# Kernel tuning notes

Hardware: AMD Instinct MI355X
Metric: run time of the kernel (lower is better)

Reference implementation:

```python
import jax, jax.numpy as jnp
import numpy as np

B, T, D, H = 2, 2048, 1024, 16
HD = D // H            # 64
FH = 2752              # SwiGLU hidden: round64(int(2*4*D/3))
BETA_INIT = 0.5


def rmsnorm(x, w, eps=1e-6):
    x32 = x.astype(jnp.float32)
    r = jax.lax.rsqrt(jnp.mean(x32 * x32, axis=-1, keepdims=True) + eps)
    return (x32 * r).astype(x.dtype) * w


def rope(x, cos, sin):
    # x: (B,H,T,HD); cos/sin: (T,HD//2)
    d2 = x.shape[-1] // 2
    x1, x2 = x[..., :d2], x[..., d2:]
    return jnp.concatenate([x1 * cos - x2 * sin, x2 * cos + x1 * sin], axis=-1)


def delta_res(x, h, gn_w, g_w, g_b, wv_w, eps_k=1e-6):
    # k-hat = normalize(h); k = k_hat / sqrt(d)
    h32 = h.astype(jnp.float32)
    nrm = jnp.sqrt(jnp.sum(h32 * h32, axis=-1, keepdims=True))
    k = (h32 / jnp.maximum(nrm, eps_k)).astype(x.dtype) * (1.0 / np.sqrt(D))
    c = rmsnorm(x, gn_w)
    logit = c @ g_w + g_b                                   # (B,T)
    beta = (2.0 * jax.nn.sigmoid(logit.astype(jnp.float32))).astype(x.dtype)[..., None]
    v = jax.nn.sigmoid(x @ wv_w)[..., None]                 # (B,T,1)
    kTx = jnp.sum(k * x, axis=-1, keepdims=True)
    return x + beta * (v - kTx) * k


def setup_inputs() -> dict:
    key = jax.random.key(0)
    ks = jax.random.split(key, 12)
    s = 0.02
    gb = np.float32(np.log(BETA_INIT / 2.0 / (1.0 - BETA_INIT / 2.0 + 1e-8)))
    return {
        "x": jax.random.normal(ks[0], (B, T, D), jnp.float32),
        "wq": jax.random.normal(ks[1], (D, D), jnp.float32) * s,
        "wk": jax.random.normal(ks[2], (D, D), jnp.float32) * s,
        "wv": jax.random.normal(ks[3], (D, D), jnp.float32) * s,
        "wo": jax.random.normal(ks[4], (D, D), jnp.float32) * s,
        "qn_w": jnp.ones((HD,), jnp.float32),
        "kn_w": jnp.ones((HD,), jnp.float32),
        "attn_norm_w": jnp.ones((D,), jnp.float32),
        "g1_norm_w": jnp.ones((D,), jnp.float32),
        "g1_w": jax.random.normal(ks[5], (D,), jnp.float32) * s,
        "g1_b": jnp.asarray(gb),
        "wv1": jax.random.normal(ks[6], (D,), jnp.float32) * s,
        "mlp_norm_w": jnp.ones((D,), jnp.float32),
        "w1": jax.random.normal(ks[7], (FH, D), jnp.float32) * s,
        "w2": jax.random.normal(ks[8], (D, FH), jnp.float32) * s,
        "w3": jax.random.normal(ks[9], (FH, D), jnp.float32) * s,
        "g2_norm_w": jnp.ones((D,), jnp.float32),
        "g2_w": jax.random.normal(ks[10], (D,), jnp.float32) * s,
        "g2_b": jnp.asarray(gb),
        "wv2": jax.random.normal(ks[11], (D,), jnp.float32) * s,
    }


def reference(x, wq, wk, wv, wo, qn_w, kn_w, attn_norm_w,
              g1_norm_w, g1_w, g1_b, wv1, mlp_norm_w, w1, w2, w3,
              g2_norm_w, g2_w, g2_b, wv2):
    # ---- attention sublayer (pre-norm) ----
    xc = rmsnorm(x, attn_norm_w)
    q = (xc @ wq.T).reshape(B, T, H, HD).swapaxes(1, 2)   # (B,H,T,HD)
    k = (xc @ wk.T).reshape(B, T, H, HD).swapaxes(1, 2)
    v = (xc @ wv.T).reshape(B, T, H, HD).swapaxes(1, 2)
    q = rmsnorm(q, qn_w)
    k = rmsnorm(k, kn_w)
    inv_freq = 1.0 / (10000.0 ** (jnp.arange(0, HD, 2, dtype=jnp.float32) / HD))
    freqs = jnp.arange(T, dtype=jnp.float32)[:, None] * inv_freq[None, :]  # (T,HD/2)
    cos, sin = jnp.cos(freqs), jnp.sin(freqs)
    q = rope(q, cos, sin)
    k = rope(k, cos, sin)
    scale = 1.0 / np.sqrt(HD)
    scores = jnp.einsum('bhqd,bhkd->bhqk', q, k) * scale
    causal = jnp.where(jnp.arange(T)[:, None] >= jnp.arange(T)[None, :], 0.0, -jnp.inf).astype(scores.dtype)
    attn = jax.nn.softmax(scores + causal, axis=-1)
    out = jnp.einsum('bhqk,bhkd->bhqd', attn, v)
    h_attn = out.swapaxes(1, 2).reshape(B, T, D) @ wo.T
    x = delta_res(x, h_attn, g1_norm_w, g1_w, g1_b, wv1)
    # ---- MLP sublayer (pre-norm SwiGLU) ----
    xm = rmsnorm(x, mlp_norm_w)
    h_mlp = (jax.nn.silu(xm @ w1.T) * (xm @ w3.T)) @ w2.T
    x = delta_res(x, h_mlp, g2_norm_w, g2_w, g2_b, wv2)
    return x
```

## Files before the change

kernel.cpp:

```cpp
#include <hip/hip_runtime.h>
#include <hip/hip_bf16.h>
#include <math.h>

using bf16 = __hip_bfloat16;
typedef __bf16 bf16x8 __attribute__((ext_vector_type(8)));
typedef float f32x4 __attribute__((ext_vector_type(4)));

static constexpr int B_ = 2, T_ = 2048, D_ = 1024, H_ = 16, HD_ = 64, FH_ = 2752;
static constexpr int BT = B_ * T_;

struct __align__(8)  bh4 { bf16 h[4]; };
struct __align__(16) bh8 { bf16 h[8]; };

#define DEV static __device__ __forceinline__

DEV float b2f(bf16 v) { return __bfloat162float(v); }
DEV bf16  f2b(float v) { return __float2bfloat16(v); }
DEV __bf16 f2bb(float f) { __hip_bfloat16 h = __float2bfloat16(f); return *reinterpret_cast<__bf16*>(&h); }
DEV float sigmoidf_(float x) { return 1.0f / (1.0f + __expf(-x)); }

DEV void load4f(const bf16* p, float* v) {
    bh4 t = *reinterpret_cast<const bh4*>(p);
#pragma unroll
    for (int i = 0; i < 4; ++i) v[i] = b2f(t.h[i]);
}
DEV void load4f(const float* p, float* v) {
    float4 t = *reinterpret_cast<const float4*>(p);
    v[0] = t.x; v[1] = t.y; v[2] = t.z; v[3] = t.w;
}
DEV void store4(float* p, const float* v) {
    float4 t; t.x = v[0]; t.y = v[1]; t.z = v[2]; t.w = v[3];
    *reinterpret_cast<float4*>(p) = t;
}
DEV float waveReduceSum(float v) {
#pragma unroll
    for (int m = 32; m; m >>= 1) v += __shfl_xor(v, m);
    return v;
}

DEV void gl_lds16(const bf16* g, bf16* lds_base) {
    __builtin_amdgcn_global_load_lds(
        (const __attribute__((address_space(1))) void*)g,
        (__attribute__((address_space(3))) void*)lds_base, 16, 0, 0);
}

__global__ __launch_bounds__(256) void k_rope_tables(float* __restrict__ cost, float* __restrict__ sint) {
    int idx = blockIdx.x * 256 + threadIdx.x;
    if (idx >= T_ * 32) return;
    int t = idx >> 5, j = idx & 31;
    float inv = powf(10000.0f, -(float)j * (1.0f / 32.0f));
    float f = (float)t * inv;
    cost[idx] = cosf(f);
    sint[idx] = sinf(f);
}

__global__ __launch_bounds__(256) void k_f2b(const float* __restrict__ in, bf16* __restrict__ out, int n8) {
    int i = blockIdx.x * 256 + threadIdx.x;
    if (i >= n8) return;
    const float4* p = reinterpret_cast<const float4*>(in + (size_t)i * 8);
    float4 a = p[0], b = p[1];
    bh8 o;
    o.h[0] = f2b(a.x); o.h[1] = f2b(a.y); o.h[2] = f2b(a.z); o.h[3] = f2b(a.w);
    o.h[4] = f2b(b.x); o.h[5] = f2b(b.y); o.h[6] = f2b(b.z); o.h[7] = f2b(b.w);
    *reinterpret_cast<bh8*>(out + (size_t)i * 8) = o;
}

__global__ __launch_bounds__(256) void k_f2b_pair(const float* __restrict__ w1, const float* __restrict__ w3,
                                                  bf16* __restrict__ outp, int n8tot) {
    int i = blockIdx.x * 256 + threadIdx.x;
    if (i >= n8tot) return;
    int r = i >> 7, c8 = i & 127;
    int sel = (r >> 4) & 1;
    int j = ((r >> 5) << 4) | (r & 15);
    const float* src = (sel ? w3 : w1) + (size_t)j * D_ + c8 * 8;
    float4 a = reinterpret_cast<const float4*>(src)[0];
    float4 b = reinterpret_cast<const float4*>(src)[1];
    bh8 o;
    o.h[0] = f2b(a.x); o.h[1] = f2b(a.y); o.h[2] = f2b(a.z); o.h[3] = f2b(a.w);
    o.h[4] = f2b(b.x); o.h[5] = f2b(b.y); o.h[6] = f2b(b.z); o.h[7] = f2b(b.w);
    *reinterpret_cast<bh8*>(outp + (size_t)r * D_ + c8 * 8) = o;
}

__global__ __launch_bounds__(256) void k_rmsnorm(const float* __restrict__ x, const float* __restrict__ w,
                                                 bf16* __restrict__ out) {
    int row = blockIdx.x, tid = threadIdx.x;
    const float* xr = x + (size_t)row * D_;
    int base = tid * 4;
    float v[4];
    load4f(xr + base, v);
    float ss = v[0]*v[0] + v[1]*v[1] + v[2]*v[2] + v[3]*v[3];
    ss = waveReduceSum(ss);
    __shared__ float red[4];
    if ((tid & 63) == 0) red[tid >> 6] = ss;
    __syncthreads();
    ss = red[0] + red[1] + red[2] + red[3];
    float r = rsqrtf(ss * (1.0f / D_) + 1e-6f);
    float wv[4];
    load4f(w + base, wv);
    bh4 o;
#pragma unroll
    for (int i = 0; i < 4; ++i) o.h[i] = f2b(v[i] * r * wv[i]);
    *reinterpret_cast<bh4*>(out + (size_t)row * D_ + base) = o;
}

template <int EPI>
__global__ __launch_bounds__(512) void k_gemm256(const bf16* __restrict__ A, const bf16* __restrict__ W,
                                                 bf16* __restrict__ C, int M, int N, int K) {
    __shared__ bf16 sA[2][256 * 32];
    __shared__ bf16 sB[2][128 * 32];
    int tid = threadIdx.x, lane = tid & 63, wid = tid >> 6;
    int m0 = blockIdx.x * 256, n0 = blockIdx.y * 128;
    int wr = wid >> 1, wc = wid & 1;
    int l16 = lane & 15, lg = lane >> 4;
    int srow = lane >> 2;
    int scol = ((lane & 3) ^ ((lane >> 3) & 3)) * 8;
    int rchunk = (lg ^ ((l16 >> 1) & 3)) * 8;

    f32x4 acc[4][4] = {};

#define STAGE(buf, k0)                                                                   \
    {                                                                                    \
        _Pragma("unroll")                                                                \
        for (int c = 0; c < 2; ++c) {                                                    \
            int r0 = wid * 32 + c * 16;                                                  \
            gl_lds16(&A[(size_t)(m0 + r0 + srow) * K + (k0) + scol], &sA[buf][r0 * 32]); \
        }                                                                                \
        {                                                                                \
            int r0 = wid * 16;                                                           \
            gl_lds16(&W[(size_t)(n0 + r0 + srow) * K + (k0) + scol], &sB[buf][r0 * 32]); \
        }                                                                                \
    }

    int nk = K >> 5;
    STAGE(0, 0);
    if (nk > 1) STAGE(1, 32);
    for (int t = 0; t < nk; ++t) {
        if (t + 1 < nk) { asm volatile("s_waitcnt vmcnt(3)" ::: "memory"); }
        else            { asm volatile("s_waitcnt vmcnt(0)" ::: "memory"); }
        __builtin_amdgcn_s_barrier();
        __builtin_amdgcn_sched_barrier(0);
        int cur = t & 1;
        bf16x8 af[4], bfr[4];
#pragma unroll
        for (int m = 0; m < 4; ++m)
            af[m] = *reinterpret_cast<const bf16x8*>(&sA[cur][(wr * 64 + m * 16 + l16) * 32 + rchunk]);
#pragma unroll
        for (int n = 0; n < 4; ++n)
            bfr[n] = *reinterpret_cast<const bf16x8*>(&sB[cur][(wc * 64 + n * 16 + l16) * 32 + rchunk]);
        __builtin_amdgcn_s_setprio(1);
#pragma unroll
        for (int m = 0; m < 4; ++m)
#pragma unroll
            for (int n = 0; n < 4; ++n)
                acc[m][n] = __builtin_amdgcn_mfma_f32_16x16x32_bf16(af[m], bfr[n], acc[m][n], 0, 0, 0);
        __builtin_amdgcn_s_setprio(0);
        __builtin_amdgcn_sched_barrier(0);
        __builtin_amdgcn_s_barrier();
        if (t + 2 < nk) STAGE(cur, (t + 2) * 32);
    }
#undef STAGE

    int rbase = m0 + wr * 64;
    if (EPI == 1) {
        int Ng = N >> 1;
        int gbase = (n0 >> 1) + wc * 32;
#pragma unroll
        for (int m = 0; m < 4; ++m) {
#pragma unroll
            for (int n2 = 0; n2 < 2; ++n2) {
                int gcol = gbase + n2 * 16 + l16;
#pragma unroll
                for (int r = 0; r < 4; ++r) {
                    int row = rbase + m * 16 + lg * 4 + r;
                    float a1 = acc[m][n2 * 2][r];
                    float a3 = acc[m][n2 * 2 + 1][r];
                    C[(size_t)row * Ng + gcol] = f2b(a1 * sigmoidf_(a1) * a3);
                }
            }
        }
    } else {
        int cbase = n0 + wc * 64;
#pragma unroll
        for (int m = 0; m < 4; ++m) {
#pragma unroll
            for (int n = 0; n < 4; ++n) {
                int col = cbase + n * 16 + l16;
#pragma unroll
                for (int r = 0; r < 4; ++r) {
                    int row = rbase + m * 16 + lg * 4 + r;
                    C[(size_t)row * N + col] = f2b(acc[m][n][r]);
                }
            }
        }
    }
}

__global__ __launch_bounds__(256) void k_gemm64(const bf16* __restrict__ A, const bf16* __restrict__ W,
                                                bf16* __restrict__ C, int M, int N, int K) {
    __shared__ bf16 sA[2][128 * 32];
    __shared__ bf16 sB[2][64 * 32];
    int tid = threadIdx.x, lane = tid & 63, wid = tid >> 6;
    int m0 = blockIdx.x * 128, n0 = blockIdx.y * 64;
    int wr = wid;
    int l16 = lane & 15, lg = lane >> 4;
    int srow = lane >> 2;
    int scol = ((lane & 3) ^ ((lane >> 3) & 3)) * 8;
    int rchunk = (lg ^ ((l16 >> 1) & 3)) * 8;

    f32x4 acc[2][4] = {};

#define STAGE(buf, k0)                                                                   \
    {                                                                                    \
        _Pragma("unroll")                                                                \
        for (int c = 0; c < 2; ++c) {                                                    \
            int r0 = wid * 32 + c * 16;                                                  \
            gl_lds16(&A[(size_t)(m0 + r0 + srow) * K + (k0) + scol], &sA[buf][r0 * 32]); \
        }                                                                                \
        {                                                                                \
            int r0 = wid * 16;                                                           \
            gl_lds16(&W[(size_t)(n0 + r0 + srow) * K + (k0) + scol], &sB[buf][r0 * 32]); \
        }                                                                                \
    }

    int nk = K >> 5;
    STAGE(0, 0);
    if (nk > 1) STAGE(1, 32);
    for (int t = 0; t < nk; ++t) {
        if (t + 1 < nk) { asm volatile("s_waitcnt vmcnt(3)" ::: "memory"); }
        else            { asm volatile("s_waitcnt vmcnt(0)" ::: "memory"); }
        __builtin_amdgcn_s_barrier();
        __builtin_amdgcn_sched_barrier(0);
        int cur = t & 1;
        bf16x8 af[2], bfr[4];
#pragma unroll
        for (int m = 0; m < 2; ++m)
            af[m] = *reinterpret_cast<const bf16x8*>(&sA[cur][(wr * 32 + m * 16 + l16) * 32 + rchunk]);
#pragma unroll
        for (int n = 0; n < 4; ++n)
            bfr[n] = *reinterpret_cast<const bf16x8*>(&sB[cur][(n * 16 + l16) * 32 + rchunk]);
        __builtin_amdgcn_s_setprio(1);
#pragma unroll
        for (int m = 0; m < 2; ++m)
#pragma unroll
            for (int n = 0; n < 4; ++n)
                acc[m][n] = __builtin_amdgcn_mfma_f32_16x16x32_bf16(af[m], bfr[n], acc[m][n], 0, 0, 0);
        __builtin_amdgcn_s_setprio(0);
        __builtin_amdgcn_sched_barrier(0);
        __builtin_amdgcn_s_barrier();
        if (t + 2 < nk) STAGE(cur, (t + 2) * 32);
    }
#undef STAGE

    int rbase = m0 + wid * 32;
#pragma unroll
    for (int m = 0; m < 2; ++m) {
#pragma unroll
        for (int n = 0; n < 4; ++n) {
            int col = n0 + n * 16 + l16;
#pragma unroll
            for (int r = 0; r < 4; ++r) {
                int row = rbase + m * 16 + lg * 4 + r;
                C[(size_t)row * N + col] = f2b(acc[m][n][r]);
            }
        }
    }
}

__global__ __launch_bounds__(256) void k_qk_norm_rope(const bf16* __restrict__ qin, const float* __restrict__ wn,
                                                      const float* __restrict__ cost, const float* __restrict__ sint,
                                                      bf16* __restrict__ qout, float scale, int ld, int off) {
    int tid = threadIdx.x;
    int g = blockIdx.x * 4 + (tid >> 6);
    int d = tid & 63;
    int h = g % H_, t = (g / H_) % T_, b = g / (H_ * T_);
    float v = b2f(qin[(size_t)(b * T_ + t) * ld + off + h * HD_ + d]);
    float ss = waveReduceSum(v * v);
    float r = rsqrtf(ss * (1.0f / HD_) + 1e-6f);
    float xn = v * r * wn[d];
    float p = __shfl_xor(xn, 32);
    float c = cost[t * 32 + (d & 31)], s = sint[t * 32 + (d & 31)];
    float o = (d < 32) ? (xn * c - p * s) : (xn * c + p * s);
    qout[((size_t)(b * H_ + h) * T_ + t) * HD_ + d] = f2b(o * scale);
}

__global__ __launch_bounds__(256) void k_v_transpose(const bf16* __restrict__ vin, bf16* __restrict__ vt,
                                                     int ld, int off) {
    __shared__ bf16 tile[64][72];
    int tid = threadIdx.x;
    int bh = blockIdx.y;
    int t0 = blockIdx.x * 64;
    int b = bh >> 4, h = bh & 15;
#pragma unroll
    for (int i = 0; i < 16; ++i) {
        int lin = i * 256 + tid;
        int tl = lin >> 6, d = lin & 63;
        tile[tl][d] = vin[(size_t)(b * T_ + t0 + tl) * ld + off + h * HD_ + d];
    }
    __syncthreads();
#pragma unroll
    for (int i = 0; i < 16; ++i) {
        int lin = i * 256 + tid;
        int d = lin >> 6, tl = lin & 63;
        vt[((size_t)bh * HD_ + d) * T_ + t0 + tl] = tile[tl][d];
    }
}

template <bool MASKED>
DEV void fa3_tile(const bf16* __restrict__ kl, const bf16* __restrict__ vl,
                  int l16, int lg, int qloc,
                  const bf16x8 qf0, const bf16x8 qf1,
                  f32x4* acc, float& m_r, float& l_r) {
    f32x4 s[8];
#pragma unroll
    for (int n = 0; n < 8; ++n) {
        int kv = n * 16 + l16;
        bf16x8 kf0 = *reinterpret_cast<const bf16x8*>(&kl[kv * 64 + (((lg ^ kv) & 7) << 3)]);
        bf16x8 kf1 = *reinterpret_cast<const bf16x8*>(&kl[kv * 64 + ((((4 + lg) ^ kv) & 7) << 3)]);
        f32x4 t = {};
        t = __builtin_amdgcn_mfma_f32_16x16x32_bf16(kf0, qf0, t, 0, 0, 0);
        t = __builtin_amdgcn_mfma_f32_16x16x32_bf16(kf1, qf1, t, 0, 0, 0);
        s[n] = t;
    }
    if (MASKED) {
#pragma unroll
        for (int n = 0; n < 8; ++n)
#pragma unroll
            for (int r = 0; r < 4; ++r)
                if (n * 16 + lg * 4 + r > qloc) s[n][r] = -INFINITY;
    }
    float mx = -INFINITY;
#pragma unroll
    for (int n = 0; n < 8; ++n)
#pragma unroll
        for (int r = 0; r < 4; ++r) mx = fmaxf(mx, s[n][r]);
    mx = fmaxf(mx, __shfl_xor(mx, 16));
    mx = fmaxf(mx, __shfl_xor(mx, 32));
    float mnew = fmaxf(m_r, mx);
    float corr = __expf(m_r - mnew);
    m_r = mnew;
    float ps = 0.0f;
#pragma unroll
    for (int n = 0; n < 8; ++n)
#pragma unroll
        for (int r = 0; r < 4; ++r) {
            float e = __expf(s[n][r] - mnew);
            s[n][r] = e;
            ps += e;
        }
    l_r = l_r * corr + ps;
#pragma unroll
    for (int np = 0; np < 4; ++np) acc[np] = acc[np] * corr;

    bf16x8 pb[4];
#pragma unroll
    for (int n2 = 0; n2 < 4; ++n2)
#pragma unroll
        for (int j = 0; j < 8; ++j)
            pb[n2][j] = f2bb(s[2 * n2 + (j >> 2)][j & 3]);

    int d15 = l16;
    int eoff = (lg & 1) * 4;
#pragma unroll
    for (int n2 = 0; n2 < 4; ++n2) {
        int c0 = (n2 * 4 + (lg >> 1));
        int c1 = c0 + 2;
#pragma unroll
        for (int np = 0; np < 4; ++np) {
            int d = np * 16 + l16;
            union { bf16x8 v; bh4 q[2]; } u;
            u.q[0] = *reinterpret_cast<const bh4*>(&vl[d * 128 + ((c0 ^ d15) << 3) + eoff]);
            u.q[1] = *reinterpret_cast<const bh4*>(&vl[d * 128 + ((c1 ^ d15) << 3) + eoff]);
            acc[np] = __builtin_amdgcn_mfma_f32_16x16x32_bf16(u.v, pb[n2], acc[np], 0, 0, 0);
        }
    }
}

__global__ __launch_bounds__(256) void k_flash(const bf16* __restrict__ Q, const bf16* __restrict__ Kk,
                                               const bf16* __restrict__ Vt, bf16* __restrict__ Out) {
    __shared__ bf16 kl[128 * 64];
    __shared__ bf16 vl[64 * 128];
    int tid = threadIdx.x, lane = tid & 63, w = tid >> 6;
    int l16 = lane & 15, lg = lane >> 4;
    int L = blockIdx.x;
    int xcd = L & 7, m = L >> 3;
    int bh = xcd * 4 + (m & 3);
    int qi = (T_ / 128 - 1) - (m >> 2);
    int q0 = qi * 128;
    int b = bh >> 4, h = bh & 15;
    const bf16* qb = Q + (size_t)bh * T_ * HD_;
    const bf16* kb = Kk + (size_t)bh * T_ * HD_;
    const bf16* vb = Vt + (size_t)bh * HD_ * T_;

    bf16x8 qfr[2][2];
#pragma unroll
    for (int f = 0; f < 2; ++f) {
        int qrow = q0 + w * 32 + f * 16 + l16;
        const bf16* qp = qb + (size_t)qrow * HD_ + lg * 8;
        qfr[f][0] = *reinterpret_cast<const bf16x8*>(qp);
        qfr[f][1] = *reinterpret_cast<const bf16x8*>(qp + 32);
    }
    f32x4 acc[2][4] = {};
    float m_r[2] = {-INFINITY, -INFINITY};
    float l_r[2] = {0.0f, 0.0f};

    for (int kv0 = 0; kv0 <= q0; kv0 += 128) {
        __syncthreads();
#pragma unroll
        for (int i = 0; i < 4; ++i) {
            int idx = i * 256 + tid;
            int kv = idx >> 3, c = idx & 7;
            *reinterpret_cast<bh8*>(&kl[kv * 64 + (((c ^ kv) & 7) << 3)]) =
                *reinterpret_cast<const bh8*>(&kb[(size_t)(kv0 + kv) * HD_ + c * 8]);
        }
#pragma unroll
        for (int i = 0; i < 4; ++i) {
            int idx = i * 256 + tid;
            int d = idx >> 4, c = idx & 15;
            *reinterpret_cast<bh8*>(&vl[d * 128 + (((c ^ d) & 15) << 3)]) =
                *reinterpret_cast<const bh8*>(&vb[(size_t)d * T_ + kv0 + c * 8]);
        }
        __syncthreads();
        if (kv0 == q0) {
#pragma unroll
            for (int f = 0; f < 2; ++f)
                fa3_tile<true>(kl, vl, l16, lg, w * 32 + f * 16 + l16,
                               qfr[f][0], qfr[f][1], acc[f], m_r[f], l_r[f]);
        } else {
#pragma unroll
            for (int f = 0; f < 2; ++f)
                fa3_tile<false>(kl, vl, l16, lg, 0,
                                qfr[f][0], qfr[f][1], acc[f], m_r[f], l_r[f]);
        }
    }
#pragma unroll
    for (int f = 0; f < 2; ++f) {
        float lt = l_r[f];
        lt += __shfl_xor(lt, 16);
        lt += __shfl_xor(lt, 32);
        float inv = 1.0f / lt;
        int qrow = q0 + w * 32 + f * 16 + l16;
#pragma unroll
        for (int np = 0; np < 4; ++np) {
            bh4 o;
#pragma unroll
            for (int r = 0; r < 4; ++r) o.h[r] = f2b(acc[f][np][r] * inv);
            *reinterpret_cast<bh4*>(&Out[(size_t)(b * T_ + qrow) * D_ + h * HD_ + np * 16 + lg * 4]) = o;
        }
    }
}

template <int WRITE_XM>
__global__ __launch_bounds__(256) void k_delta_res(const float* __restrict__ x, const bf16* __restrict__ h,
                                                   const float* __restrict__ gn_w, const float* __restrict__ g_w,
                                                   const float* __restrict__ g_b, const float* __restrict__ wv_w,
                                                   float* __restrict__ out,
                                                   bf16* __restrict__ xm_out, const float* __restrict__ mlp_w) {
    int row = blockIdx.x, tid = threadIdx.x;
    int base = tid * 4;
    float xv[4], hv[4], gnv[4], gwv[4], wvv[4];
    load4f(x + (size_t)row * D_ + base, xv);
    load4f(h + (size_t)row * D_ + base, hv);
    load4f(gn_w + base, gnv);
    load4f(g_w + base, gwv);
    load4f(wv_w + base, wvv);
    float s_h2 = 0, s_x2 = 0, s_xg = 0, s_xv = 0, s_hx = 0;
#pragma unroll
    for (int i = 0; i < 4; ++i) {
        s_h2 += hv[i] * hv[i];
        s_x2 += xv[i] * xv[i];
        s_xg += xv[i] * gnv[i] * gwv[i];
        s_xv += xv[i] * wvv[i];
        s_hx += hv[i] * xv[i];
    }
    s_h2 = waveReduceSum(s_h2); s_x2 = waveReduceSum(s_x2); s_xg = waveReduceSum(s_xg);
    s_xv = waveReduceSum(s_xv); s_hx = waveReduceSum(s_hx);
    __shared__ float red[4][5];
    int wid = tid >> 6;
    if ((tid & 63) == 0) {
        red[wid][0] = s_h2; red[wid][1] = s_x2; red[wid][2] = s_xg;
        red[wid][3] = s_xv; red[wid][4] = s_hx;
    }
    __syncthreads();
    s_h2 = red[0][0] + red[1][0] + red[2][0] + red[3][0];
    s_x2 = red[0][1] + red[1][1] + red[2][1] + red[3][1];
    s_xg = red[0][2] + red[1][2] + red[2][2] + red[3][2];
    s_xv = red[0][3] + red[1][3] + red[2][3] + red[3][3];
    s_hx = red[0][4] + red[1][4] + red[2][4] + red[3][4];

    float r = rsqrtf(s_x2 * (1.0f / D_) + 1e-6f);
    float logit = r * s_xg + g_b[0];
    float beta = 2.0f * sigmoidf_(logit);
    float vsig = sigmoidf_(s_xv);
    float nrm = sqrtf(s_h2);
    float ks = (1.0f / 32.0f) / fmaxf(nrm, 1e-6f);
    float coef = beta * (vsig - ks * s_hx) * ks;
    float o[4];
#pragma unroll
    for (int i = 0; i < 4; ++i) o[i] = xv[i] + coef * hv[i];
    store4(out + (size_t)row * D_ + base, o);

    if (WRITE_XM) {
        float s2 = o[0]*o[0] + o[1]*o[1] + o[2]*o[2] + o[3]*o[3];
        s2 = waveReduceSum(s2);
        __shared__ float red2[4];
        __syncthreads();
        if ((tid & 63) == 0) red2[wid] = s2;
        __syncthreads();
        s2 = red2[0] + red2[1] + red2[2] + red2[3];
        float rr = rsqrtf(s2 * (1.0f / D_) + 1e-6f);
        float mw[4];
        load4f(mlp_w + base, mw);
        bh4 ob;
#pragma unroll
        for (int i = 0; i < 4; ++i) ob.h[i] = f2b(o[i] * rr * mw[i]);
        *reinterpret_cast<bh4*>(xm_out + (size_t)row * D_ + base) = ob;
    }
}

extern "C" void kernel_launch(void* const* d_in, const int* in_sizes, int n_in,
                              void* d_out, int out_size, void* d_ws, size_t ws_size,
                              hipStream_t stream) {
    const float* x       = (const float*)d_in[0];
    const float* wq      = (const float*)d_in[1];
    const float* wk      = (const float*)d_in[2];
    const float* wv      = (const float*)d_in[3];
    const float* wo      = (const float*)d_in[4];
    const float* qn_w    = (const float*)d_in[5];
    const float* kn_w    = (const float*)d_in[6];
    const float* attn_nw = (const float*)d_in[7];
    const float* g1_nw   = (const float*)d_in[8];
    const float* g1_w    = (const float*)d_in[9];
    const float* g1_b    = (const float*)d_in[10];
    const float* wv1     = (const float*)d_in[11];
    const float* mlp_nw  = (const float*)d_in[12];
    const float* w1      = (const float*)d_in[13];
    const float* w2      = (const float*)d_in[14];
    const float* w3      = (const float*)d_in[15];
    const float* g2_nw   = (const float*)d_in[16];
    const float* g2_w    = (const float*)d_in[17];
    const float* g2_b    = (const float*)d_in[18];
    const float* wv2     = (const float*)d_in[19];
    float* out = (float*)d_out;

    char* ws = (char*)d_ws;
    const size_t KB = 1024;
    const size_t MB = 1024 * 1024;
    float* cost = (float*)(ws);
    float* sint = (float*)(ws + 256 * KB);
    bf16* XC = (bf16*)(ws + 512 * KB);
    bf16* Bb = (bf16*)(ws + 512 * KB + 8  * MB);
    bf16* Cb = (bf16*)(ws + 512 * KB + 16 * MB);
    bf16* Db = (bf16*)(ws + 512 * KB + 24 * MB);
    bf16* Eb = (bf16*)(ws + 512 * KB + 32 * MB);
    bf16* Fb = (bf16*)(ws + 512 * KB + 40 * MB);
    bf16* Gb = (bf16*)(ws + 512 * KB + 48 * MB);
    float* x1 = (float*)(ws + 512 * KB + 56 * MB);

    bf16* wqkv = Eb;
    bf16* qkv  = Bb;
    bf16* wbo  = XC;
    bf16* attn_out = Bb;
    bf16* wpair = Bb;
    bf16* w2b  = Db;
    bf16* g    = Eb;
    bf16* hmlp = XC;

    const int nDD = D_ * D_ / 8, nFD = FH_ * D_ / 8;
    dim3 blk(256);

    k_rope_tables<<<dim3((T_ * 32) / 256), blk, 0, stream>>>(cost, sint);

    k_rmsnorm<<<dim3(BT), blk, 0, stream>>>(x, attn_nw, XC);
    k_f2b<<<dim3((nDD + 255) / 256), blk, 0, stream>>>(wq, wqkv, nDD);
    k_f2b<<<dim3((nDD + 255) / 256), blk, 0, stream>>>(wk, wqkv + (size_t)D_ * D_, nDD);
    k_f2b<<<dim3((nDD + 255) / 256), blk, 0, stream>>>(wv, wqkv + (size_t)2 * D_ * D_, nDD);

    k_gemm256<0><<<dim3(16, 24), dim3(512), 0, stream>>>(XC, wqkv, qkv, BT, 3 * D_, D_);

    k_qk_norm_rope<<<dim3(BT * H_ / 4), blk, 0, stream>>>(qkv, qn_w, cost, sint, Eb, 0.125f, 3 * D_, 0);
    k_qk_norm_rope<<<dim3(BT * H_ / 4), blk, 0, stream>>>(qkv, kn_w, cost, sint, Fb, 1.0f, 3 * D_, D_);
    k_v_transpose<<<dim3(T_ / 64, B_ * H_), blk, 0, stream>>>(qkv, Gb, 3 * D_, 2 * D_);

    k_f2b<<<dim3((nDD + 255) / 256), blk, 0, stream>>>(wo, wbo, nDD);
    k_flash<<<dim3((T_ / 128) * B_ * H_), blk, 0, stream>>>(Eb, Fb, Gb, attn_out);

    k_gemm64<<<dim3(32, 16), blk, 0, stream>>>(attn_out, wbo, Cb, BT, D_, D_);

    k_delta_res<1><<<dim3(BT), blk, 0, stream>>>(x, Cb, g1_nw, g1_w, g1_b, wv1, x1, XC, mlp_nw);

    k_f2b_pair<<<dim3((2 * nFD + 255) / 256), blk, 0, stream>>>(w1, w3, wpair, 2 * nFD);
    k_f2b<<<dim3((nFD + 255) / 256), blk, 0, stream>>>(w2, w2b, nFD);

    k_gemm256<1><<<dim3(16, 43), dim3(512), 0, stream>>>(XC, wpair, g, BT, 2 * FH_, D_);

    k_gemm64<<<dim3(32, 16), blk, 0, stream>>>(g, w2b, hmlp, BT, D_, FH_);

    k_delta_res<0><<<dim3(BT), blk, 0, stream>>>(x1, hmlp, g2_nw, g2_w, g2_b, wv2, out, nullptr, nullptr);
}
```

Before: 282.5 us.

## Retile wide GEMM to 128x256 tiles with 4 waves and pad MLP hidden dim

```diff
diff --git a/kernel.cpp b/kernel.cpp
--- a/kernel.cpp
+++ b/kernel.cpp
@@ -8,6 +8,7 @@
 
 static constexpr int B_ = 2, T_ = 2048, D_ = 1024, H_ = 16, HD_ = 64, FH_ = 2752;
 static constexpr int BT = B_ * T_;
+static constexpr int FHP = 2816;
 
 struct __align__(8)  bh4 { bf16 h[4]; };
 struct __align__(16) bh8 { bf16 h[8]; };
@@ -72,6 +73,7 @@
     int r = i >> 7, c8 = i & 127;
     int sel = (r >> 4) & 1;
     int j = ((r >> 5) << 4) | (r & 15);
+    if (j > FH_ - 1) j = FH_ - 1;
     const float* src = (sel ? w3 : w1) + (size_t)j * D_ + c8 * 8;
     float4 a = reinterpret_cast<const float4*>(src)[0];
     float4 b = reinterpret_cast<const float4*>(src)[1];
@@ -104,19 +106,18 @@
 }
 
 template <int EPI>
-__global__ __launch_bounds__(512) void k_gemm256(const bf16* __restrict__ A, const bf16* __restrict__ W,
-                                                 bf16* __restrict__ C, int M, int N, int K) {
-    __shared__ bf16 sA[2][256 * 32];
-    __shared__ bf16 sB[2][128 * 32];
+__global__ __launch_bounds__(256) void k_gemmW(const bf16* __restrict__ A, const bf16* __restrict__ W,
+                                               bf16* __restrict__ C, int M, int N, int K) {
+    __shared__ bf16 sA[2][128 * 32];
+    __shared__ bf16 sB[2][256 * 32];
     int tid = threadIdx.x, lane = tid & 63, wid = tid >> 6;
-    int m0 = blockIdx.x * 256, n0 = blockIdx.y * 128;
-    int wr = wid >> 1, wc = wid & 1;
+    int m0 = blockIdx.x * 128, n0 = blockIdx.y * 256;
     int l16 = lane & 15, lg = lane >> 4;
     int srow = lane >> 2;
     int scol = ((lane & 3) ^ ((lane >> 3) & 3)) * 8;
     int rchunk = (lg ^ ((l16 >> 1) & 3)) * 8;
 
-    f32x4 acc[4][4] = {};
+    f32x4 acc[8][4] = {};
 
 #define STAGE(buf, k0)                                                                   \
     {                                                                                    \
@@ -125,8 +126,9 @@
             int r0 = wid * 32 + c * 16;                                                  \
             gl_lds16(&A[(size_t)(m0 + r0 + srow) * K + (k0) + scol], &sA[buf][r0 * 32]); \
         }                                                                                \
-        {                                                                                \
-            int r0 = wid * 16;                                                           \
+        _Pragma("unroll")                                                                \
+        for (int c = 0; c < 4; ++c) {                                                    \
+            int r0 = wid * 64 + c * 16;                                                  \
             gl_lds16(&W[(size_t)(n0 + r0 + srow) * K + (k0) + scol], &sB[buf][r0 * 32]); \
         }                                                                                \
     }
@@ -135,59 +137,63 @@
     STAGE(0, 0);
     if (nk > 1) STAGE(1, 32);
     for (int t = 0; t < nk; ++t) {
-        if (t + 1 < nk) { asm volatile("s_waitcnt vmcnt(3)" ::: "memory"); }
+        if (t + 1 < nk) { asm volatile("s_waitcnt vmcnt(6)" ::: "memory"); }
         else            { asm volatile("s_waitcnt vmcnt(0)" ::: "memory"); }
         __builtin_amdgcn_s_barrier();
         __builtin_amdgcn_sched_barrier(0);
         int cur = t & 1;
-        bf16x8 af[4], bfr[4];
-#pragma unroll
-        for (int m = 0; m < 4; ++m)
-            af[m] = *reinterpret_cast<const bf16x8*>(&sA[cur][(wr * 64 + m * 16 + l16) * 32 + rchunk]);
+        bf16x8 bfr[4];
 #pragma unroll
         for (int n = 0; n < 4; ++n)
-            bfr[n] = *reinterpret_cast<const bf16x8*>(&sB[cur][(wc * 64 + n * 16 + l16) * 32 + rchunk]);
-        __builtin_amdgcn_s_setprio(1);
-#pragma unroll
-        for (int m = 0; m < 4; ++m)
-#pragma unroll
-            for (int n = 0; n < 4; ++n)
-                acc[m][n] = __builtin_amdgcn_mfma_f32_16x16x32_bf16(af[m], bfr[n], acc[m][n], 0, 0, 0);
-        __builtin_amdgcn_s_setprio(0);
+            bfr[n] = *reinterpret_cast<const bf16x8*>(&sB[cur][(wid * 64 + n * 16 + l16) * 32 + rchunk]);
+#pragma unroll
+        for (int mh = 0; mh < 2; ++mh) {
+            bf16x8 af[4];
+#pragma unroll
+            for (int m = 0; m < 4; ++m)
+                af[m] = *reinterpret_cast<const bf16x8*>(&sA[cur][((mh * 4 + m) * 16 + l16) * 32 + rchunk]);
+            __builtin_amdgcn_s_setprio(1);
+#pragma unroll
+            for (int m = 0; m < 4; ++m)
+#pragma unroll
+                for (int n = 0; n < 4; ++n)
+                    acc[mh * 4 + m][n] = __builtin_amdgcn_mfma_f32_16x16x32_bf16(af[m], bfr[n], acc[mh * 4 + m][n], 0, 0, 0);
+            __builtin_amdgcn_s_setprio(0);
+        }
         __builtin_amdgcn_sched_barrier(0);
         __builtin_amdgcn_s_barrier();
         if (t + 2 < nk) STAGE(cur, (t + 2) * 32);
     }
 #undef STAGE
 
-    int rbase = m0 + wr * 64;
     if (EPI == 1) {
-        int Ng = N >> 1;
-        int gbase = (n0 >> 1) + wc * 32;
-#pragma unroll
-        for (int m = 0; m < 4; ++m) {
+        int gbase = (n0 >> 1) + wid * 32;
+#pragma unroll
+        for (int m = 0; m < 8; ++m) {
 #pragma unroll
             for (int n2 = 0; n2 < 2; ++n2) {
                 int gcol = gbase + n2 * 16 + l16;
-#pragma unroll
-                for (int r = 0; r < 4; ++r) {
-                    int row = rbase + m * 16 + lg * 4 + r;
-                    float a1 = acc[m][n2 * 2][r];
-                    float a3 = acc[m][n2 * 2 + 1][r];
-                    C[(size_t)row * Ng + gcol] = f2b(a1 * sigmoidf_(a1) * a3);
+                if (gcol < FH_) {
+#pragma unroll
+                    for (int r = 0; r < 4; ++r) {
+                        int row = m0 + m * 16 + lg * 4 + r;
+                        float a1 = acc[m][n2 * 2][r];
+                        float a3 = acc[m][n2 * 2 + 1][r];
+                        C[(size_t)row * FH_ + gcol] = f2b(a1 * sigmoidf_(a1) * a3);
+                    }
                 }
             }
         }
     } else {
-        int cbase = n0 + wc * 64;
-#pragma unroll
-        for (int m = 0; m < 4; ++m) {
+        int cbase = n0 + wid * 64;
+#pragma unroll
+        for (int m = 0; m < 8; ++m) {
 #pragma unroll
             for (int n = 0; n < 4; ++n) {
                 int col = cbase + n * 16 + l16;
 #pragma unroll
                 for (int r = 0; r < 4; ++r) {
-                    int row = rbase + m * 16 + lg * 4 + r;
+                    int row = m0 + m * 16 + lg * 4 + r;
                     C[(size_t)row * N + col] = f2b(acc[m][n][r]);
                 }
             }
@@ -575,7 +581,7 @@
     k_f2b<<<dim3((nDD + 255) / 256), blk, 0, stream>>>(wk, wqkv + (size_t)D_ * D_, nDD);
     k_f2b<<<dim3((nDD + 255) / 256), blk, 0, stream>>>(wv, wqkv + (size_t)2 * D_ * D_, nDD);
 
-    k_gemm256<0><<<dim3(16, 24), dim3(512), 0, stream>>>(XC, wqkv, qkv, BT, 3 * D_, D_);
+    k_gemmW<0><<<dim3(32, 12), blk, 0, stream>>>(XC, wqkv, qkv, BT, 3 * D_, D_);
 
     k_qk_norm_rope<<<dim3(BT * H_ / 4), blk, 0, stream>>>(qkv, qn_w, cost, sint, Eb, 0.125f, 3 * D_, 0);
     k_qk_norm_rope<<<dim3(BT * H_ / 4), blk, 0, stream>>>(qkv, kn_w, cost, sint, Fb, 1.0f, 3 * D_, D_);
@@ -588,10 +594,11 @@
 
     k_delta_res<1><<<dim3(BT), blk, 0, stream>>>(x, Cb, g1_nw, g1_w, g1_b, wv1, x1, XC, mlp_nw);
 
-    k_f2b_pair<<<dim3((2 * nFD + 255) / 256), blk, 0, stream>>>(w1, w3, wpair, 2 * nFD);
+    int n8pair = 2 * FHP * D_ / 8;
+    k_f2b_pair<<<dim3((n8pair + 255) / 256), blk, 0, stream>>>(w1, w3, wpair, n8pair);
     k_f2b<<<dim3((nFD + 255) / 256), blk, 0, stream>>>(w2, w2b, nFD);
 
-    k_gemm256<1><<<dim3(16, 43), dim3(512), 0, stream>>>(XC, wpair, g, BT, 2 * FH_, D_);
+    k_gemmW<1><<<dim3(32, 2 * FHP / 256), blk, 0, stream>>>(XC, wpair, g, BT, 2 * FHP, D_);
 
     k_gemm64<<<dim3(32, 16), blk, 0, stream>>>(g, w2b, hmlp, BT, D_, FH_);
 
```

Result: slower. 345.4 us (+22.3%).
